# Performance work log

Measured on AMD Instinct MI355X. Metric: run time of the kernel, lower is better.

The kernel has to match this reference:

```python
import jax, jax.numpy as jnp
import numpy as np

KERNEL_LIST = (4, 8)
STRIDE = 4
EXT = 1
NUM_HEADS = 4
KEY_DIM = 32   # head_dim * attn_ratio = 64 * 0.5
HEAD_DIM = 64
SCALE = KEY_DIM ** -0.5


def _pool_matrix(inp, out):
    # torch adaptive_avg_pool2d: window i covers [floor(i*inp/out), ceil((i+1)*inp/out))
    P = np.zeros((out, inp), np.float32)
    for i in range(out):
        s0 = (i * inp) // out
        e0 = -((-(i + 1) * inp) // out)
        P[i, s0:e0] = 1.0 / (e0 - s0)
    return jnp.asarray(P)


def _dwconv3(x, w, b):
    # depthwise 3x3 conv, padding 1 (groups == channels)
    y = jax.lax.conv_general_dilated(
        x, w, window_strides=(1, 1), padding=((1, 1), (1, 1)),
        feature_group_count=x.shape[1],
        dimension_numbers=("NCHW", "OIHW", "NCHW"))
    return y + b[None, :, None, None]


def _attention(x, qkv_w, qkv_b, proj_w, proj_b, pe_w, pe_b):
    B, C, H, W = x.shape
    N = H * W
    qkv = jnp.einsum("oc,bchw->bohw", qkv_w, x) + qkv_b[None, :, None, None]
    qkv = qkv.reshape(B, NUM_HEADS, 2 * KEY_DIM + HEAD_DIM, N)
    q = qkv[:, :, :KEY_DIM]                # (B,h,kd,N)
    k = qkv[:, :, KEY_DIM:2 * KEY_DIM]     # (B,h,kd,N)
    v = qkv[:, :, 2 * KEY_DIM:]            # (B,h,hd,N)
    attn = jax.nn.softmax(jnp.einsum("bhkn,bhkm->bhnm", q, k) * SCALE, axis=-1)
    # v @ attn^T : out[d,n] = sum_m v[d,m] * attn[n,m]
    o = jnp.einsum("bhdm,bhnm->bhdn", v, attn).reshape(B, C, H, W)
    o = o + _dwconv3(v.reshape(B, C, H, W), pe_w, pe_b)
    return jnp.einsum("oc,bchw->bohw", proj_w, o) + proj_b[None, :, None, None]


def _extract(xp, Kp, s):
    # overlapping patches; layout (N, C, Lh, Kp, Lw, Kp); window order is (lh, lw)
    N, C, Hp, Wp = xp.shape
    Lh = (Hp - Kp) // s + 1
    Lw = (Wp - Kp) // s + 1
    hi = jnp.arange(Lh)[:, None] * s + jnp.arange(Kp)[None, :]  # (Lh, Kp)
    wi = jnp.arange(Lw)[:, None] * s + jnp.arange(Kp)[None, :]
    p = xp[:, :, hi, :]          # (N, C, Lh, Kp, Wp)
    p = p[:, :, :, :, wi]        # (N, C, Lh, Kp, Lw, Kp)
    return p, Lh, Lw


def setup_inputs() -> dict:
    key = jax.random.key(0)
    ks = jax.random.split(key, 9)
    C = 256
    w = 0.02
    return {
        "x": jax.random.normal(ks[0], (8, C, 64, 64), jnp.float32),
        "qkv_w": jax.random.normal(ks[1], (512, C), jnp.float32) * w,
        "qkv_b": jax.random.normal(ks[2], (512,), jnp.float32) * w,
        "proj_w": jax.random.normal(ks[3], (C, C), jnp.float32) * w,
        "proj_b": jax.random.normal(ks[4], (C,), jnp.float32) * w,
        "attn_pe_w": jax.random.normal(ks[5], (C, 1, 3, 3), jnp.float32) * w,
        "attn_pe_b": jax.random.normal(ks[6], (C,), jnp.float32) * w,
        "dp_pe_w": jax.random.normal(ks[7], (C, 1, 3, 3), jnp.float32) * w,
        "dp_pe_b": jax.random.normal(ks[8], (C,), jnp.float32) * w,
    }


def reference(x, qkv_w, qkv_b, proj_w, proj_b, attn_pe_w, attn_pe_b, dp_pe_w, dp_pe_b):
    N, C, H, W = x.shape
    xp = jnp.pad(x, ((0, 0), (0, 0), (EXT, EXT), (EXT, EXT)), mode="edge")  # replicate pad
    outs = [x]
    for K in KERNEL_LIST:
        Kp = K + 2 * EXT
        p, Lh, Lw = _extract(xp, Kp, STRIDE)
        P = _pool_matrix(Kp, K)
        # adaptive avg pool Kp->K on both spatial dims; windows ordered (lh, lw)
        pooled = jnp.einsum("pi,ncaibj,qj->nabcpq", P, p, P)
        pooled = pooled.reshape(N * Lh * Lw, C, K, K)
        y = _dwconv3(pooled, dp_pe_w, dp_pe_b) + pooled
        a = _attention(y, qkv_w, qkv_b, proj_w, proj_b, attn_pe_w, attn_pe_b)
        # torch does a raw .view(N, C*K*K, L) on the (N*L, C, K, K) buffer
        cols = a.reshape(N, C, K, K, Lh, Lw)
        cols_p = cols.transpose(0, 1, 2, 4, 3, 5)  # (N, C, K, Lh, K, Lw)
        hh = jnp.arange(Lh)[None, :] * STRIDE + jnp.arange(K)[:, None]  # (K, Lh)
        ww = jnp.arange(Lw)[None, :] * STRIDE + jnp.arange(K)[:, None]  # (K, Lw)
        folded = jnp.zeros((N, C, H, W), x.dtype).at[
            :, :, hh[:, :, None, None], ww[None, None, :, :]].add(cols_p)
        count = jnp.zeros((1, 1, H, W), x.dtype).at[
            :, :, hh[:, :, None, None], ww[None, None, :, :]].add(
            jnp.ones((1, 1, K, Lh, K, Lw), x.dtype))
        outs.append(folded / count)
    return sum(outs) / len(outs)
```

## Files before the change

kernel.cpp:

```cpp
#include <hip/hip_runtime.h>
#include <hip/hip_bf16.h>

typedef __bf16 bf16x8 __attribute__((ext_vector_type(8)));
typedef float  f32x4  __attribute__((ext_vector_type(4)));

#define DEV static __device__ __forceinline__

DEV float bf2f(ushort u) { unsigned x = ((unsigned)u) << 16; return __uint_as_float(x); }
DEV ushort f2bf(float f) {
    __bf16 b = (__bf16)f;
    return __builtin_bit_cast(ushort, b);
}

typedef __attribute__((address_space(1))) const unsigned int gu32;
typedef __attribute__((address_space(3))) unsigned int lu32;
DEV void gload16(const ushort* g, ushort* l) {
    __builtin_amdgcn_global_load_lds((gu32*)g, (lu32*)l, 16, 0, 0);
}

__global__ __launch_bounds__(256) void prep_kernel(
    const float* __restrict__ qkv_w, const float* __restrict__ proj_w,
    const float* __restrict__ apw,
    ushort* __restrict__ qw_bf, ushort* __restrict__ pw_bf, ushort* __restrict__ wt)
{
    int bid = blockIdx.x;
    if (bid < 128) {
        int i = (bid * 256 + threadIdx.x) * 4;
        float4 v = *(const float4*)(qkv_w + i);
        ushort4 o;
        o.x = f2bf(v.x); o.y = f2bf(v.y); o.z = f2bf(v.z); o.w = f2bf(v.w);
        *(ushort4*)(qw_bf + i) = o;
    } else if (bid < 192) {
        int i = ((bid - 128) * 256 + threadIdx.x) * 4;
        float4 v = *(const float4*)(proj_w + i);
        ushort4 o;
        o.x = f2bf(v.x); o.y = f2bf(v.y); o.z = f2bf(v.z); o.w = f2bf(v.w);
        *(ushort4*)(pw_bf + i) = o;
    } else {
        int i = (bid - 192) * 256 + threadIdx.x;
        if (i < 9 * 256) {
            int tap = i >> 8, c = i & 255;
            wt[i] = f2bf(apw[c * 9 + tap]);
        }
    }
}

__global__ __launch_bounds__(256) void box_kernel(
    const float* __restrict__ x,
    ushort* __restrict__ B)
{
    int br = blockIdx.x % 65; int g = blockIdx.x / 65;
    const float* xg = x + (size_t)g * 256 * 4096;
    ushort* Bg = B + (size_t)g * 65 * 65 * 256;
    const int r0 = max(br - 1, 0) * 64;
    const int r1 = min(br, 63) * 64;
    __shared__ float s[128][65];
    const int wl = threadIdx.x & 63, cq = threadIdx.x >> 6;
    const int c2 = threadIdx.x & 127, bh = threadIdx.x >> 7;
    for (int half = 0; half < 2; ++half) {
#pragma unroll 4
        for (int it = 0; it < 32; ++it) {
            int cl_ = it * 4 + cq;
            const float* xp = xg + (size_t)(half * 128 + cl_) * 4096;
            s[cl_][wl] = xp[r0 + wl] + xp[r1 + wl];
        }
        __syncthreads();
        for (int bc = bh; bc < 65; bc += 2) {
            float v = 0.25f * (s[c2][max(bc - 1, 0)] + s[c2][min(bc, 63)]);
            Bg[((size_t)br * 65 + bc) * 256 + half * 128 + c2] = f2bf(v);
        }
        __syncthreads();
    }
}

template<int K, int L>
__global__ __launch_bounds__(256) void pool_kernel(
    const ushort* __restrict__ B,
    const float* __restrict__ w9,
    const float* __restrict__ bias,
    ushort* __restrict__ y)
{
    constexpr int HF = K / 2;
    const int pk = blockIdx.x;
    const int lw = pk % L; int t = pk / L; const int lh = t % L; const int g = t / L;
    const int c = threadIdx.x;
    const ushort* Bg = B + (size_t)g * 65 * 65 * 256 + c;
    float pool[K][K];
#pragma unroll
    for (int p = 0; p < K; ++p) {
        const int br = lh * 4 + p + (p >= HF ? 1 : 0);
#pragma unroll
        for (int q = 0; q < K; ++q) {
            const int bc = lw * 4 + q + (q >= HF ? 1 : 0);
            pool[p][q] = bf2f(Bg[((size_t)br * 65 + bc) * 256]);
        }
    }
    float wv[9];
#pragma unroll
    for (int i = 0; i < 9; ++i) wv[i] = w9[c * 9 + i];
    const float bv = bias[c];
    ushort* yp = y + (size_t)pk * (K * K) * 256 + c;
#pragma unroll
    for (int p = 0; p < K; ++p) {
#pragma unroll
        for (int q = 0; q < K; ++q) {
            float a = pool[p][q] + bv;
#pragma unroll
            for (int dp = -1; dp <= 1; ++dp) {
#pragma unroll
                for (int dq = -1; dq <= 1; ++dq) {
                    int pp = p + dp, qq = q + dq;
                    if (pp >= 0 && pp < K && qq >= 0 && qq < K)
                        a += wv[(dp + 1) * 3 + (dq + 1)] * pool[pp][qq];
                }
            }
            yp[(p * K + q) * 256] = f2bf(a);
        }
    }
}

template<int OC, int EPI, int K, int L, int RT>
__global__ __launch_bounds__(256) void gemm_kernel(
    const ushort* __restrict__ act,
    const ushort* __restrict__ w,
    const float* __restrict__ bias,
    ushort* __restrict__ out_bf)
{
    __shared__ __attribute__((aligned(16))) ushort As[128][32];
    __shared__ __attribute__((aligned(16))) ushort Ws[128][32];
    constexpr int NT = OC / 128;
    const int id  = blockIdx.x;
    const int xc  = id & 7;
    const int ctb = (id >> 3) % NT;
    const int tt  = id / (8 * NT);
    const int rowt = tt * 8 + xc;
    if (rowt >= RT) return;
    const int tid  = threadIdx.x;
    const int n0   = rowt * 128;
    const int ch0  = ctb * 128;
    const int wv   = tid >> 6, lane = tid & 63;
    const int l15  = lane & 15, quad = lane >> 4;
    const int wm   = wv >> 1, wn = wv & 1;

    const int qlog = (lane & 3) ^ ((lane >> 3) & 3);
    const size_t soff = (size_t)(lane >> 2) * 256 + (size_t)qlog * 8;
    const ushort* aS0 = act + ((size_t)n0 + wv * 32) * 256 + soff;
    const ushort* wS0 = w   + ((size_t)ch0 + wv * 32) * 256 + soff;
    const ushort* aS1 = aS0 + 16 * 256;
    const ushort* wS1 = wS0 + 16 * 256;
    ushort* aD0 = &As[wv * 32][0];
    ushort* wD0 = &Ws[wv * 32][0];
    ushort* aD1 = aD0 + 16 * 32;
    ushort* wD1 = wD0 + 16 * 32;

    const int rcol = (quad ^ ((l15 >> 1) & 3)) * 8;
    f32x4 acc[4][4] = {};
    for (int k0 = 0; k0 < 256; k0 += 32) {
        gload16(aS0 + k0, aD0);
        gload16(aS1 + k0, aD1);
        gload16(wS0 + k0, wD0);
        gload16(wS1 + k0, wD1);
        __syncthreads();
        bf16x8 af[4], bw[4];
#pragma unroll
        for (int t = 0; t < 4; ++t) {
            af[t] = *(const bf16x8*)&As[wm * 64 + t * 16 + l15][rcol];
            bw[t] = *(const bf16x8*)&Ws[wn * 64 + t * 16 + l15][rcol];
        }
#pragma unroll
        for (int mt = 0; mt < 4; ++mt)
#pragma unroll
            for (int nt = 0; nt < 4; ++nt)
                acc[mt][nt] = __builtin_amdgcn_mfma_f32_16x16x32_bf16(af[mt], bw[nt], acc[mt][nt], 0, 0, 0);
        __syncthreads();
    }

    float bv[4];
#pragma unroll
    for (int nt = 0; nt < 4; ++nt) bv[nt] = bias[ch0 + wn * 64 + nt * 16 + l15];
#pragma unroll
    for (int mt = 0; mt < 4; ++mt) {
#pragma unroll
        for (int r = 0; r < 4; ++r) {
            const int n = n0 + wm * 64 + mt * 16 + quad * 4 + r;
            if (EPI == 0) {
                ushort* dst = out_bf + (size_t)n * OC + ch0 + wn * 64;
#pragma unroll
                for (int nt = 0; nt < 4; ++nt)
                    dst[nt * 16 + l15] = f2bf(acc[mt][nt][r] + bv[nt]);
            } else {
                constexpr int K2 = K * K;
                constexpr int LL = L * L;
                const int b_g   = n >> (K == 8 ? 6 : 4);
                const int pq    = n & (K2 - 1);
                const int gl    = b_g / LL;
                const int b_loc = b_g - gl * LL;
                const size_t base = (size_t)gl * (256 * K2 * LL) + (size_t)b_loc * 256 * K2 + pq;
#pragma unroll
                for (int nt = 0; nt < 4; ++nt) {
                    const int ch = ch0 + wn * 64 + nt * 16 + l15;
                    out_bf[base + (size_t)ch * K2] = f2bf(acc[mt][nt][r] + bv[nt]);
                }
            }
        }
    }
}

__global__ __launch_bounds__(128, 4) void attn8_mfma_kernel(
    const ushort* __restrict__ qkv,
    const ushort* __restrict__ wt,
    const float* __restrict__ pe_b,
    ushort* __restrict__ o_out)
{
    constexpr float SCALE = 0.17677669529663687f;
    __shared__ __attribute__((aligned(16))) ushort PB[64][72];
    __shared__ __attribute__((aligned(16))) ushort Vt[64][72];
    __shared__ __attribute__((aligned(16))) ushort wsh[9][64];
    __shared__ float bsh[64];
    const int tid  = threadIdx.x;
    const int lane = tid & 63;
    const int ww   = tid >> 6;
    const int b    = blockIdx.x >> 2;
    const int h    = blockIdx.x & 3;
    const int cbase = h * 64;
    const int l15  = lane & 15, quad = lane >> 4;
    const ushort* base = qkv + (size_t)b * 64 * 512 + h * 128;

    if (lane < 36) {
        int tap = lane >> 2, c8 = (lane & 3) * 8;
        *(uint4*)&wsh[tap][ww * 32 + c8] = *(const uint4*)&wt[tap * 256 + cbase + ww * 32 + c8];
    }
    if (lane < 32) bsh[ww * 32 + lane] = pe_b[cbase + ww * 32 + lane];

    {
        const int m = lane;
        const ushort* vsrc = base + (size_t)m * 512 + 64 + ww * 32;
        const int d0 = ww * 32;
#pragma unroll
        for (int t = 0; t < 4; ++t) {
            uint4 vv = *(const uint4*)(vsrc + t * 8);
            unsigned u[4] = {vv.x, vv.y, vv.z, vv.w};
#pragma unroll
            for (int e = 0; e < 4; ++e) {
                Vt[d0 + t * 8 + e * 2][m]     = (ushort)(u[e] & 0xFFFF);
                Vt[d0 + t * 8 + e * 2 + 1][m] = (ushort)(u[e] >> 16);
            }
        }
    }

    bf16x8 fq[2];
#pragma unroll
    for (int s = 0; s < 2; ++s) {
        int n = (ww + 2 * s) * 16 + l15;
        fq[s] = *(const bf16x8*)(base + (size_t)n * 512 + quad * 8);
    }
    f32x4 S[2][4];
    __builtin_amdgcn_s_setprio(1);
#pragma unroll
    for (int mt = 0; mt < 4; ++mt) {
        int m = mt * 16 + l15;
        bf16x8 fk = *(const bf16x8*)(base + (size_t)m * 512 + 32 + quad * 8);
#pragma unroll
        for (int s = 0; s < 2; ++s) {
            f32x4 z = {0.f, 0.f, 0.f, 0.f};
            S[s][mt] = __builtin_amdgcn_mfma_f32_16x16x32_bf16(fq[s], fk, z, 0, 0, 0);
        }
    }
    __builtin_amdgcn_s_setprio(0);

    {
        const int d   = ww * 32 + (lane & 31);
        const int pb4 = (lane >> 5) * 4;
        float wreg[9];
#pragma unroll
        for (int i = 0; i < 9; ++i) wreg[i] = bf2f(wsh[i][d]);
        const float bias0 = bsh[d];
#pragma unroll
        for (int it = 0; it < 4; ++it) {
            const int p = pb4 + it;
            float pe[8];
#pragma unroll
            for (int q = 0; q < 8; ++q) pe[q] = bias0;
#pragma unroll
            for (int dpi = 0; dpi < 3; ++dpi) {
                const int pp = p + dpi - 1;
                if (pp >= 0 && pp < 8) {
                    bf16x8 v8 = *(const bf16x8*)&Vt[d][pp * 8];
                    float v[8];
#pragma unroll
                    for (int e = 0; e < 8; ++e) v[e] = (float)v8[e];
                    const float w0 = wreg[dpi * 3], w1 = wreg[dpi * 3 + 1], w2 = wreg[dpi * 3 + 2];
                    pe[0] += w1 * v[0] + w2 * v[1];
#pragma unroll
                    for (int q = 1; q < 7; ++q) pe[q] += w0 * v[q - 1] + w1 * v[q] + w2 * v[q + 1];
                    pe[7] += w0 * v[6] + w1 * v[7];
                }
            }
            ushort pk[8];
#pragma unroll
            for (int e = 0; e < 8; ++e) pk[e] = f2bf(pe[e]);
            *(uint4*)&PB[d][p * 8] = *(const uint4*)pk;
        }
    }
    __syncthreads();

    f32x4 O[2][4];
#pragma unroll
    for (int s = 0; s < 2; ++s)
#pragma unroll
        for (int dt = 0; dt < 4; ++dt) {
            ushort4 t4 = *(const ushort4*)&PB[dt * 16 + l15][(ww + 2 * s) * 16 + quad * 4];
            O[s][dt][0] = bf2f(t4.x);
            O[s][dt][1] = bf2f(t4.y);
            O[s][dt][2] = bf2f(t4.z);
            O[s][dt][3] = bf2f(t4.w);
        }

#pragma unroll
    for (int s = 0; s < 2; ++s) {
#pragma unroll
        for (int r = 0; r < 4; ++r) {
            float mx = -1e30f;
#pragma unroll
            for (int mt = 0; mt < 4; ++mt) { S[s][mt][r] *= SCALE; mx = fmaxf(mx, S[s][mt][r]); }
            mx = fmaxf(mx, __shfl_xor(mx, 1));
            mx = fmaxf(mx, __shfl_xor(mx, 2));
            mx = fmaxf(mx, __shfl_xor(mx, 4));
            mx = fmaxf(mx, __shfl_xor(mx, 8));
            float sum = 0.f;
#pragma unroll
            for (int mt = 0; mt < 4; ++mt) { float e = __expf(S[s][mt][r] - mx); S[s][mt][r] = e; sum += e; }
            sum += __shfl_xor(sum, 1);
            sum += __shfl_xor(sum, 2);
            sum += __shfl_xor(sum, 4);
            sum += __shfl_xor(sum, 8);
            float inv = 1.f / sum;
#pragma unroll
            for (int mt = 0; mt < 4; ++mt) S[s][mt][r] *= inv;
        }
    }
    __syncthreads();

#pragma unroll
    for (int s = 0; s < 2; ++s)
#pragma unroll
        for (int r = 0; r < 4; ++r) {
            int n = (ww + 2 * s) * 16 + quad * 4 + r;
#pragma unroll
            for (int mt = 0; mt < 4; ++mt)
                PB[n][mt * 16 + l15] = f2bf(S[s][mt][r]);
        }

#pragma unroll
    for (int ks = 0; ks < 2; ++ks) {
        bf16x8 fp[2], fv[4];
#pragma unroll
        for (int s = 0; s < 2; ++s)
            fp[s] = *(const bf16x8*)&PB[(ww + 2 * s) * 16 + l15][ks * 32 + quad * 8];
#pragma unroll
        for (int dt = 0; dt < 4; ++dt)
            fv[dt] = *(const bf16x8*)&Vt[dt * 16 + l15][ks * 32 + quad * 8];
        __builtin_amdgcn_s_setprio(1);
#pragma unroll
        for (int s = 0; s < 2; ++s)
#pragma unroll
            for (int dt = 0; dt < 4; ++dt)
                O[s][dt] = __builtin_amdgcn_mfma_f32_16x16x32_bf16(fp[s], fv[dt], O[s][dt], 0, 0, 0);
        __builtin_amdgcn_s_setprio(0);
    }

#pragma unroll
    for (int s = 0; s < 2; ++s)
#pragma unroll
        for (int r = 0; r < 4; ++r) {
            int n = (ww + 2 * s) * 16 + quad * 4 + r;
#pragma unroll
            for (int dt = 0; dt < 4; ++dt)
                PB[n][dt * 16 + l15] = f2bf(O[s][dt][r]);
        }
#pragma unroll
    for (int it = 0; it < 4; ++it) {
        int cidx = it * 64 + lane;
        int rl = cidx >> 3, c8 = (cidx & 7) * 8;
        int row = ww * 16 + (rl & 15) + (rl >> 4) * 32;
        uint4 v = *(const uint4*)&PB[row][c8];
        *(uint4*)(o_out + (size_t)(b * 64 + row) * 256 + cbase + c8) = v;
    }
}

__global__ __launch_bounds__(256) void attn4_mfma_kernel(
    const ushort* __restrict__ qkv,
    const ushort* __restrict__ wt,
    const float* __restrict__ pe_b,
    ushort* __restrict__ o_out)
{
    constexpr float SCALE = 0.17677669529663687f;
    __shared__ __attribute__((aligned(16))) ushort wsh[9][256];
    __shared__ float bsh[256];
    __shared__ __attribute__((aligned(16))) ushort Vt4[4][64][32];
    __shared__ __attribute__((aligned(16))) ushort VP[4][16][64];
    __shared__ __attribute__((aligned(16))) ushort Pm[4][16][32];
    const int tid  = threadIdx.x;
    const int lane = tid & 63;
    const int w    = tid >> 6;
    const int b    = blockIdx.x;
    const int h    = w;
    const int cbase = h * 64;
    const int l15  = lane & 15, quad = lane >> 4;
    const ushort* base = qkv + (size_t)b * 16 * 512 + h * 128;

    for (int i = tid; i < 9 * 32; i += 256) {
        int tap = i >> 5, c8 = (i & 31) * 8;
        *(uint4*)&wsh[tap][c8] = *(const uint4*)&wt[tap * 256 + c8];
    }
    bsh[tid] = pe_b[tid];
    __syncthreads();

    {
        uint4 z = {0u, 0u, 0u, 0u};
#pragma unroll
        for (int t = 0; t < 4; ++t)
            *(uint4*)&Vt4[w][t * 16 + (lane >> 2)][(lane & 3) * 8] = z;
        *(uint4*)&Pm[w][lane >> 2][(lane & 3) * 8] = z;
    }

    {
        const int m = lane & 15, dblk = lane >> 4;
        const ushort* vsrc = base + (size_t)m * 512 + 64 + dblk * 16;
        uint4 v0 = *(const uint4*)(vsrc);
        uint4 v1 = *(const uint4*)(vsrc + 8);
        *(uint4*)&VP[w][m][dblk * 16]     = v0;
        *(uint4*)&VP[w][m][dblk * 16 + 8] = v1;
        ushort us[16];
        *(uint4*)&us[0] = v0; *(uint4*)&us[8] = v1;
        const int mb = m >> 3, m7 = m & 7;
#pragma unroll
        for (int e = 0; e < 16; ++e) {
            int d = dblk * 16 + e;
            Vt4[w][d][((mb ^ (d & 3)) << 3) + m7] = us[e];
        }
    }

    bf16x8 fq = *(const bf16x8*)(base + (size_t)l15 * 512 + quad * 8);
    bf16x8 fk = *(const bf16x8*)(base + (size_t)l15 * 512 + 32 + quad * 8);
    f32x4 z4 = {0.f, 0.f, 0.f, 0.f};
    f32x4 S = __builtin_amdgcn_mfma_f32_16x16x32_bf16(fq, fk, z4, 0, 0, 0);

    float p[4];
#pragma unroll
    for (int r = 0; r < 4; ++r) {
        float v = S[r] * SCALE;
        float mx = v;
        mx = fmaxf(mx, __shfl_xor(mx, 1));
        mx = fmaxf(mx, __shfl_xor(mx, 2));
        mx = fmaxf(mx, __shfl_xor(mx, 4));
        mx = fmaxf(mx, __shfl_xor(mx, 8));
        float e = __expf(v - mx);
        float sum = e;
        sum += __shfl_xor(sum, 1);
        sum += __shfl_xor(sum, 2);
        sum += __shfl_xor(sum, 4);
        sum += __shfl_xor(sum, 8);
        p[r] = e / sum;
    }
#pragma unroll
    for (int r = 0; r < 4; ++r) {
        int n = quad * 4 + r;
        Pm[w][n][(((l15 >> 3) ^ (n & 3)) << 3) + (l15 & 7)] = f2bf(p[r]);
    }

    float pe[2][8];
    const int n_ = lane & 15;
    const int pp0 = n_ >> 2, qq0 = n_ & 3;
#pragma unroll
    for (int it = 0; it < 2; ++it) {
        int ch = (lane >> 4) + it * 4;
#pragma unroll
        for (int e = 0; e < 8; ++e) pe[it][e] = bsh[cbase + ch * 8 + e];
    }
#pragma unroll
    for (int tap = 0; tap < 9; ++tap) {
        const int dp = tap / 3 - 1, dq = tap % 3 - 1;
        const int pp = pp0 + dp, qq = qq0 + dq;
        if (pp >= 0 && pp < 4 && qq >= 0 && qq < 4) {
            const int mm = pp * 4 + qq;
#pragma unroll
            for (int it = 0; it < 2; ++it) {
                int ch = (lane >> 4) + it * 4;
                uint4 wv4 = *(const uint4*)&wsh[tap][cbase + ch * 8];
                uint4 vv  = *(const uint4*)&VP[w][mm][ch * 8];
                unsigned uw[4] = {wv4.x, wv4.y, wv4.z, wv4.w};
                unsigned uv[4] = {vv.x, vv.y, vv.z, vv.w};
#pragma unroll
                for (int e2 = 0; e2 < 4; ++e2) {
                    float wlo = __uint_as_float(uw[e2] << 16);
                    float whi = __uint_as_float(uw[e2] & 0xFFFF0000u);
                    float vlo = __uint_as_float(uv[e2] << 16);
                    float vhi = __uint_as_float(uv[e2] & 0xFFFF0000u);
                    pe[it][2 * e2]     += wlo * vlo;
                    pe[it][2 * e2 + 1] += whi * vhi;
                }
            }
        }
    }
#pragma unroll
    for (int it = 0; it < 2; ++it) {
        int ch = (lane >> 4) + it * 4;
        ushort pk[8];
#pragma unroll
        for (int e = 0; e < 8; ++e) pk[e] = f2bf(pe[it][e]);
        *(uint4*)&VP[w][n_][ch * 8] = *(const uint4*)pk;
    }

    f32x4 O[4];
#pragma unroll
    for (int dt = 0; dt < 4; ++dt)
#pragma unroll
        for (int r = 0; r < 4; ++r)
            O[dt][r] = bf2f(VP[w][quad * 4 + r][dt * 16 + l15]);

    bf16x8 fp = *(const bf16x8*)&Pm[w][l15][((quad ^ (l15 & 3)) << 3)];
    __builtin_amdgcn_s_setprio(1);
#pragma unroll
    for (int dt = 0; dt < 4; ++dt) {
        bf16x8 fv = *(const bf16x8*)&Vt4[w][dt * 16 + l15][((quad ^ (l15 & 3)) << 3)];
        O[dt] = __builtin_amdgcn_mfma_f32_16x16x32_bf16(fp, fv, O[dt], 0, 0, 0);
    }
    __builtin_amdgcn_s_setprio(0);

#pragma unroll
    for (int dt = 0; dt < 4; ++dt)
#pragma unroll
        for (int r = 0; r < 4; ++r)
            VP[w][quad * 4 + r][dt * 16 + l15] = f2bf(O[dt][r]);

#pragma unroll
    for (int j = 0; j < 2; ++j) {
        int idx = j * 64 + lane;
        int row = idx >> 3, c8 = (idx & 7) * 8;
        uint4 v = *(const uint4*)&VP[w][row][c8];
        *(uint4*)(o_out + (size_t)(b * 16 + row) * 256 + cbase + c8) = v;
    }
}

__global__ __launch_bounds__(256) void final_kernel(
    const float* __restrict__ x,
    const ushort* __restrict__ s8,
    const ushort* __restrict__ s4,
    float* __restrict__ out)
{
    __shared__ __attribute__((aligned(16))) ushort l8[14400];
    __shared__ __attribute__((aligned(16))) ushort l4[4096];
    const int c2 = blockIdx.x & 255;
    const int g  = blockIdx.x >> 8;
    const int tid = threadIdx.x;
    const ushort* s8g = s8 + (size_t)g * (256 * 64 * 225) + (size_t)c2 * 14400;
    const ushort* s4g = s4 + (size_t)g * (256 * 16 * 256) + (size_t)c2 * 4096;
#pragma unroll
    for (int i = 0; i < 8; ++i) {
        int idx = i * 256 + tid;
        if (idx < 1800) *(uint4*)&l8[idx * 8] = *(const uint4*)&s8g[idx * 8];
    }
#pragma unroll
    for (int i = 0; i < 2; ++i) {
        int idx = i * 256 + tid;
        *(uint4*)&l4[idx * 8] = *(const uint4*)&s4g[idx * 8];
    }
    __syncthreads();
    const float third = 1.f / 3.f;
    const size_t gc_off = ((size_t)(g * 256 + c2)) * 4096;
#pragma unroll
    for (int it = 0; it < 4; ++it) {
        int pix0 = it * 1024 + tid * 4;
        int h = pix0 >> 6, w0 = pix0 & 63;
        int lh_lo = (h >= 8) ? ((h - 4) >> 2) : 0, lh_hi = min(14, h >> 2);
        float4 xv = *(const float4*)(x + gc_off + pix0);
        float xa[4] = {xv.x, xv.y, xv.z, xv.w};
        float o4[4];
#pragma unroll
        for (int j = 0; j < 4; ++j) {
            int w = w0 + j;
            int lw_lo = (w >= 8) ? ((w - 4) >> 2) : 0, lw_hi = min(14, w >> 2);
            float v4 = bf2f(l4[(((h & 3) * 4 + (w & 3)) * 16 + (h >> 2)) * 16 + (w >> 2)]);
            float v8 = 0.f;
            for (int lh2 = lh_lo; lh2 <= lh_hi; ++lh2) {
                int p2 = h - lh2 * 4;
                for (int lw2 = lw_lo; lw2 <= lw_hi; ++lw2) {
                    int q2 = w - lw2 * 4;
                    v8 += bf2f(l8[((p2 * 8 + q2) * 15 + lh2) * 15 + lw2]);
                }
            }
            float inv = 1.f / (float)((lh_hi - lh_lo + 1) * (lw_hi - lw_lo + 1));
            o4[j] = (xa[j] + v8 * inv + v4) * third;
        }
        float4 ov = {o4[0], o4[1], o4[2], o4[3]};
        *(float4*)(out + gc_off + pix0) = ov;
    }
}

extern "C" void kernel_launch(void* const* d_in, const int* in_sizes, int n_in,
                              void* d_out, int out_size, void* d_ws, size_t ws_size,
                              hipStream_t stream)
{
    const float* x      = (const float*)d_in[0];
    const float* qkv_w  = (const float*)d_in[1];
    const float* qkv_b  = (const float*)d_in[2];
    const float* proj_w = (const float*)d_in[3];
    const float* proj_b = (const float*)d_in[4];
    const float* apw    = (const float*)d_in[5];
    const float* apb    = (const float*)d_in[6];
    const float* dpw    = (const float*)d_in[7];
    const float* dpb    = (const float*)d_in[8];
    float* out = (float*)d_out;

    const size_t S8_B = 8ull * 225 * 256 * 64 * 2;
    const size_t S4_B = 8ull * 256 * 256 * 16 * 2;
    const size_t W_B  = (512ull * 256 + 256ull * 256 + 9ull * 256) * 2;
    const size_t B_B  = 8ull * 65 * 65 * 256 * 2;
    const size_t Y1_B = 8ull * 14400 * 256 * 2;
    const size_t Q1_B = 8ull * 14400 * 512 * 2;
    const size_t Y2_B = 4ull * 14400 * 256 * 2;
    const size_t Q2_B = 4ull * 14400 * 512 * 2;

    const bool onepass = ws_size >= S8_B + S4_B + Y1_B + Q1_B + W_B + B_B;
    const size_t Y_B = onepass ? Y1_B : Y2_B;
    const size_t Q_B = onepass ? Q1_B : Q2_B;
    if (!onepass && ws_size < S8_B + S4_B + Y2_B + Q2_B + W_B + B_B) {
        hipMemsetAsync(d_out, 0x46, 4, stream);
        return;
    }
    ushort* s8    = (ushort*)d_ws;
    ushort* s4    = s8 + S8_B / 2;
    ushort* ybuf  = s4 + S4_B / 2;
    ushort* qbuf  = ybuf + Y_B / 2;
    ushort* qw_bf = qbuf + Q_B / 2;
    ushort* pw_bf = qw_bf + 512 * 256;
    ushort* wt    = pw_bf + 256 * 256;
    ushort* Bbuf  = (ushort*)((char*)d_ws + S8_B + S4_B + Y_B + Q_B + W_B);

    prep_kernel<<<201, 256, 0, stream>>>(qkv_w, proj_w, apw, qw_bf, pw_bf, wt);
    box_kernel<<<8 * 65, 256, 0, stream>>>(x, Bbuf);

    if (onepass) {
        pool_kernel<8, 15><<<8 * 225, 256, 0, stream>>>(Bbuf, dpw, dpb, ybuf);
        gemm_kernel<512, 0, 8, 15, 900><<<113 * 8 * 4, 256, 0, stream>>>(ybuf, qw_bf, qkv_b, qbuf);
        attn8_mfma_kernel<<<1800 * 4, 128, 0, stream>>>(qbuf, wt, apb, ybuf);
        gemm_kernel<256, 1, 8, 15, 900><<<113 * 8 * 2, 256, 0, stream>>>(ybuf, pw_bf, proj_b, s8);
    } else {
        for (int hf = 0; hf < 2; ++hf) {
            ushort* B_h = Bbuf + (size_t)hf * 4 * 65 * 65 * 256;
            ushort* s8_h = s8 + (size_t)hf * 4 * 225 * 256 * 64;
            pool_kernel<8, 15><<<4 * 225, 256, 0, stream>>>(B_h, dpw, dpb, ybuf);
            gemm_kernel<512, 0, 8, 15, 450><<<57 * 8 * 4, 256, 0, stream>>>(ybuf, qw_bf, qkv_b, qbuf);
            attn8_mfma_kernel<<<900 * 4, 128, 0, stream>>>(qbuf, wt, apb, ybuf);
            gemm_kernel<256, 1, 8, 15, 450><<<57 * 8 * 2, 256, 0, stream>>>(ybuf, pw_bf, proj_b, s8_h);
        }
    }
    pool_kernel<4, 16><<<8 * 256, 256, 0, stream>>>(Bbuf, dpw, dpb, ybuf);
    gemm_kernel<512, 0, 4, 16, 256><<<32 * 8 * 4, 256, 0, stream>>>(ybuf, qw_bf, qkv_b, qbuf);
    attn4_mfma_kernel<<<2048, 256, 0, stream>>>(qbuf, wt, apb, ybuf);
    gemm_kernel<256, 1, 4, 16, 256><<<32 * 8 * 2, 256, 0, stream>>>(ybuf, pw_bf, proj_b, s4);

    final_kernel<<<2048, 256, 0, stream>>>(x, s8, s4, out);
}
```

Measured before the change: 360.3 us.

## Process two patches per attn8 block and prefetch second patch's inputs

Each attn8 block now handles two patch-batches (bp and bp+phalf), halving the grid. The global loads of Q, K and V for the second patch are issued right after the first patch's QK MFMAs, so their latency overlaps with the first patch's depthwise conv, softmax and PV work. In exchange the block needs more registers for the prefetched fragments, has fewer blocks to spread across CUs, and adds an extra barrier between the two iterations.

```diff
diff --git a/kernel.cpp b/kernel.cpp
--- a/kernel.cpp
+++ b/kernel.cpp
@@ -210,7 +210,8 @@
     const ushort* __restrict__ qkv,
     const ushort* __restrict__ wt,
     const float* __restrict__ pe_b,
-    ushort* __restrict__ o_out)
+    ushort* __restrict__ o_out,
+    int phalf)
 {
     constexpr float SCALE = 0.17677669529663687f;
     __shared__ __attribute__((aligned(16))) ushort PB[64][72];
@@ -220,11 +221,10 @@
     const int tid  = threadIdx.x;
     const int lane = tid & 63;
     const int ww   = tid >> 6;
-    const int b    = blockIdx.x >> 2;
+    const int bp   = blockIdx.x >> 2;
     const int h    = blockIdx.x & 3;
     const int cbase = h * 64;
     const int l15  = lane & 15, quad = lane >> 4;
-    const ushort* base = qkv + (size_t)b * 64 * 512 + h * 128;
 
     if (lane < 36) {
         int tap = lane >> 2, c8 = (lane & 3) * 8;
@@ -232,159 +232,191 @@
     }
     if (lane < 32) bsh[ww * 32 + lane] = pe_b[cbase + ww * 32 + lane];
 
+    uint4  vr[4];
+    bf16x8 fq[2];
+    bf16x8 fk[4];
     {
-        const int m = lane;
-        const ushort* vsrc = base + (size_t)m * 512 + 64 + ww * 32;
-        const int d0 = ww * 32;
-#pragma unroll
-        for (int t = 0; t < 4; ++t) {
-            uint4 vv = *(const uint4*)(vsrc + t * 8);
-            unsigned u[4] = {vv.x, vv.y, vv.z, vv.w};
-#pragma unroll
-            for (int e = 0; e < 4; ++e) {
-                Vt[d0 + t * 8 + e * 2][m]     = (ushort)(u[e] & 0xFFFF);
-                Vt[d0 + t * 8 + e * 2 + 1][m] = (ushort)(u[e] >> 16);
-            }
-        }
-    }
-
-    bf16x8 fq[2];
-#pragma unroll
-    for (int s = 0; s < 2; ++s) {
-        int n = (ww + 2 * s) * 16 + l15;
-        fq[s] = *(const bf16x8*)(base + (size_t)n * 512 + quad * 8);
-    }
-    f32x4 S[2][4];
-    __builtin_amdgcn_s_setprio(1);
-#pragma unroll
-    for (int mt = 0; mt < 4; ++mt) {
-        int m = mt * 16 + l15;
-        bf16x8 fk = *(const bf16x8*)(base + (size_t)m * 512 + 32 + quad * 8);
+        const ushort* base0 = qkv + (size_t)bp * 64 * 512 + h * 128;
+        const ushort* vsrc = base0 + (size_t)lane * 512 + 64 + ww * 32;
+#pragma unroll
+        for (int t = 0; t < 4; ++t) vr[t] = *(const uint4*)(vsrc + t * 8);
 #pragma unroll
         for (int s = 0; s < 2; ++s) {
-            f32x4 z = {0.f, 0.f, 0.f, 0.f};
-            S[s][mt] = __builtin_amdgcn_mfma_f32_16x16x32_bf16(fq[s], fk, z, 0, 0, 0);
-        }
-    }
-    __builtin_amdgcn_s_setprio(0);
-
-    {
-        const int d   = ww * 32 + (lane & 31);
-        const int pb4 = (lane >> 5) * 4;
-        float wreg[9];
-#pragma unroll
-        for (int i = 0; i < 9; ++i) wreg[i] = bf2f(wsh[i][d]);
-        const float bias0 = bsh[d];
+            int n = (ww + 2 * s) * 16 + l15;
+            fq[s] = *(const bf16x8*)(base0 + (size_t)n * 512 + quad * 8);
+        }
+#pragma unroll
+        for (int mt = 0; mt < 4; ++mt) {
+            int m = mt * 16 + l15;
+            fk[mt] = *(const bf16x8*)(base0 + (size_t)m * 512 + 32 + quad * 8);
+        }
+    }
+
+#pragma unroll
+    for (int j = 0; j < 2; ++j) {
+        const int b = (j == 0) ? bp : bp + phalf;
+        if (j == 1) __syncthreads();
+
+        {
+            const int m = lane, d0 = ww * 32;
+#pragma unroll
+            for (int t = 0; t < 4; ++t) {
+                unsigned u[4] = {vr[t].x, vr[t].y, vr[t].z, vr[t].w};
+#pragma unroll
+                for (int e = 0; e < 4; ++e) {
+                    Vt[d0 + t * 8 + e * 2][m]     = (ushort)(u[e] & 0xFFFF);
+                    Vt[d0 + t * 8 + e * 2 + 1][m] = (ushort)(u[e] >> 16);
+                }
+            }
+        }
+
+        f32x4 S[2][4];
+        __builtin_amdgcn_s_setprio(1);
+#pragma unroll
+        for (int mt = 0; mt < 4; ++mt) {
+#pragma unroll
+            for (int s = 0; s < 2; ++s) {
+                f32x4 z = {0.f, 0.f, 0.f, 0.f};
+                S[s][mt] = __builtin_amdgcn_mfma_f32_16x16x32_bf16(fq[s], fk[mt], z, 0, 0, 0);
+            }
+        }
+        __builtin_amdgcn_s_setprio(0);
+
+        if (j == 0) {
+            const ushort* base1 = qkv + (size_t)(bp + phalf) * 64 * 512 + h * 128;
+            const ushort* vsrc = base1 + (size_t)lane * 512 + 64 + ww * 32;
+#pragma unroll
+            for (int t = 0; t < 4; ++t) vr[t] = *(const uint4*)(vsrc + t * 8);
+#pragma unroll
+            for (int s = 0; s < 2; ++s) {
+                int n = (ww + 2 * s) * 16 + l15;
+                fq[s] = *(const bf16x8*)(base1 + (size_t)n * 512 + quad * 8);
+            }
+#pragma unroll
+            for (int mt = 0; mt < 4; ++mt) {
+                int m = mt * 16 + l15;
+                fk[mt] = *(const bf16x8*)(base1 + (size_t)m * 512 + 32 + quad * 8);
+            }
+        }
+
+        {
+            const int d   = ww * 32 + (lane & 31);
+            const int pb4 = (lane >> 5) * 4;
+            float wreg[9];
+#pragma unroll
+            for (int i = 0; i < 9; ++i) wreg[i] = bf2f(wsh[i][d]);
+            const float bias0 = bsh[d];
+#pragma unroll
+            for (int it = 0; it < 4; ++it) {
+                const int p = pb4 + it;
+                float pe[8];
+#pragma unroll
+                for (int q = 0; q < 8; ++q) pe[q] = bias0;
+#pragma unroll
+                for (int dpi = 0; dpi < 3; ++dpi) {
+                    const int pp = p + dpi - 1;
+                    if (pp >= 0 && pp < 8) {
+                        bf16x8 v8 = *(const bf16x8*)&Vt[d][pp * 8];
+                        float v[8];
+#pragma unroll
+                        for (int e = 0; e < 8; ++e) v[e] = (float)v8[e];
+                        const float w0 = wreg[dpi * 3], w1 = wreg[dpi * 3 + 1], w2 = wreg[dpi * 3 + 2];
+                        pe[0] += w1 * v[0] + w2 * v[1];
+#pragma unroll
+                        for (int q = 1; q < 7; ++q) pe[q] += w0 * v[q - 1] + w1 * v[q] + w2 * v[q + 1];
+                        pe[7] += w0 * v[6] + w1 * v[7];
+                    }
+                }
+                ushort pk[8];
+#pragma unroll
+                for (int e = 0; e < 8; ++e) pk[e] = f2bf(pe[e]);
+                *(uint4*)&PB[d][p * 8] = *(const uint4*)pk;
+            }
+        }
+        __syncthreads();
+
+        f32x4 O[2][4];
+#pragma unroll
+        for (int s = 0; s < 2; ++s)
+#pragma unroll
+            for (int dt = 0; dt < 4; ++dt) {
+                ushort4 t4 = *(const ushort4*)&PB[dt * 16 + l15][(ww + 2 * s) * 16 + quad * 4];
+                O[s][dt][0] = bf2f(t4.x);
+                O[s][dt][1] = bf2f(t4.y);
+                O[s][dt][2] = bf2f(t4.z);
+                O[s][dt][3] = bf2f(t4.w);
+            }
+
+#pragma unroll
+        for (int s = 0; s < 2; ++s) {
+#pragma unroll
+            for (int r = 0; r < 4; ++r) {
+                float mx = -1e30f;
+#pragma unroll
+                for (int mt = 0; mt < 4; ++mt) { S[s][mt][r] *= SCALE; mx = fmaxf(mx, S[s][mt][r]); }
+                mx = fmaxf(mx, __shfl_xor(mx, 1));
+                mx = fmaxf(mx, __shfl_xor(mx, 2));
+                mx = fmaxf(mx, __shfl_xor(mx, 4));
+                mx = fmaxf(mx, __shfl_xor(mx, 8));
+                float sum = 0.f;
+#pragma unroll
+                for (int mt = 0; mt < 4; ++mt) { float e = __expf(S[s][mt][r] - mx); S[s][mt][r] = e; sum += e; }
+                sum += __shfl_xor(sum, 1);
+                sum += __shfl_xor(sum, 2);
+                sum += __shfl_xor(sum, 4);
+                sum += __shfl_xor(sum, 8);
+                float inv = 1.f / sum;
+#pragma unroll
+                for (int mt = 0; mt < 4; ++mt) S[s][mt][r] *= inv;
+            }
+        }
+        __syncthreads();
+
+#pragma unroll
+        for (int s = 0; s < 2; ++s)
+#pragma unroll
+            for (int r = 0; r < 4; ++r) {
+                int n = (ww + 2 * s) * 16 + quad * 4 + r;
+#pragma unroll
+                for (int mt = 0; mt < 4; ++mt)
+                    PB[n][mt * 16 + l15] = f2bf(S[s][mt][r]);
+            }
+
+#pragma unroll
+        for (int ks = 0; ks < 2; ++ks) {
+            bf16x8 fp[2], fv[4];
+#pragma unroll
+            for (int s = 0; s < 2; ++s)
+                fp[s] = *(const bf16x8*)&PB[(ww + 2 * s) * 16 + l15][ks * 32 + quad * 8];
+#pragma unroll
+            for (int dt = 0; dt < 4; ++dt)
+                fv[dt] = *(const bf16x8*)&Vt[dt * 16 + l15][ks * 32 + quad * 8];
+            __builtin_amdgcn_s_setprio(1);
+#pragma unroll
+            for (int s = 0; s < 2; ++s)
+#pragma unroll
+                for (int dt = 0; dt < 4; ++dt)
+                    O[s][dt] = __builtin_amdgcn_mfma_f32_16x16x32_bf16(fp[s], fv[dt], O[s][dt], 0, 0, 0);
+            __builtin_amdgcn_s_setprio(0);
+        }
+
+#pragma unroll
+        for (int s = 0; s < 2; ++s)
+#pragma unroll
+            for (int r = 0; r < 4; ++r) {
+                int n = (ww + 2 * s) * 16 + quad * 4 + r;
+#pragma unroll
+                for (int dt = 0; dt < 4; ++dt)
+                    PB[n][dt * 16 + l15] = f2bf(O[s][dt][r]);
+            }
 #pragma unroll
         for (int it = 0; it < 4; ++it) {
-            const int p = pb4 + it;
-            float pe[8];
-#pragma unroll
-            for (int q = 0; q < 8; ++q) pe[q] = bias0;
-#pragma unroll
-            for (int dpi = 0; dpi < 3; ++dpi) {
-                const int pp = p + dpi - 1;
-                if (pp >= 0 && pp < 8) {
-                    bf16x8 v8 = *(const bf16x8*)&Vt[d][pp * 8];
-                    float v[8];
-#pragma unroll
-                    for (int e = 0; e < 8; ++e) v[e] = (float)v8[e];
-                    const float w0 = wreg[dpi * 3], w1 = wreg[dpi * 3 + 1], w2 = wreg[dpi * 3 + 2];
-                    pe[0] += w1 * v[0] + w2 * v[1];
-#pragma unroll
-                    for (int q = 1; q < 7; ++q) pe[q] += w0 * v[q - 1] + w1 * v[q] + w2 * v[q + 1];
-                    pe[7] += w0 * v[6] + w1 * v[7];
-                }
-            }
-            ushort pk[8];
-#pragma unroll
-            for (int e = 0; e < 8; ++e) pk[e] = f2bf(pe[e]);
-            *(uint4*)&PB[d][p * 8] = *(const uint4*)pk;
-        }
-    }
-    __syncthreads();
-
-    f32x4 O[2][4];
-#pragma unroll
-    for (int s = 0; s < 2; ++s)
-#pragma unroll
-        for (int dt = 0; dt < 4; ++dt) {
-            ushort4 t4 = *(const ushort4*)&PB[dt * 16 + l15][(ww + 2 * s) * 16 + quad * 4];
-            O[s][dt][0] = bf2f(t4.x);
-            O[s][dt][1] = bf2f(t4.y);
-            O[s][dt][2] = bf2f(t4.z);
-            O[s][dt][3] = bf2f(t4.w);
-        }
-
-#pragma unroll
-    for (int s = 0; s < 2; ++s) {
-#pragma unroll
-        for (int r = 0; r < 4; ++r) {
-            float mx = -1e30f;
-#pragma unroll
-            for (int mt = 0; mt < 4; ++mt) { S[s][mt][r] *= SCALE; mx = fmaxf(mx, S[s][mt][r]); }
-            mx = fmaxf(mx, __shfl_xor(mx, 1));
-            mx = fmaxf(mx, __shfl_xor(mx, 2));
-            mx = fmaxf(mx, __shfl_xor(mx, 4));
-            mx = fmaxf(mx, __shfl_xor(mx, 8));
-            float sum = 0.f;
-#pragma unroll
-            for (int mt = 0; mt < 4; ++mt) { float e = __expf(S[s][mt][r] - mx); S[s][mt][r] = e; sum += e; }
-            sum += __shfl_xor(sum, 1);
-            sum += __shfl_xor(sum, 2);
-            sum += __shfl_xor(sum, 4);
-            sum += __shfl_xor(sum, 8);
-            float inv = 1.f / sum;
-#pragma unroll
-            for (int mt = 0; mt < 4; ++mt) S[s][mt][r] *= inv;
-        }
-    }
-    __syncthreads();
-
-#pragma unroll
-    for (int s = 0; s < 2; ++s)
-#pragma unroll
-        for (int r = 0; r < 4; ++r) {
-            int n = (ww + 2 * s) * 16 + quad * 4 + r;
-#pragma unroll
-            for (int mt = 0; mt < 4; ++mt)
-                PB[n][mt * 16 + l15] = f2bf(S[s][mt][r]);
-        }
-
-#pragma unroll
-    for (int ks = 0; ks < 2; ++ks) {
-        bf16x8 fp[2], fv[4];
-#pragma unroll
-        for (int s = 0; s < 2; ++s)
-            fp[s] = *(const bf16x8*)&PB[(ww + 2 * s) * 16 + l15][ks * 32 + quad * 8];
-#pragma unroll
-        for (int dt = 0; dt < 4; ++dt)
-            fv[dt] = *(const bf16x8*)&Vt[dt * 16 + l15][ks * 32 + quad * 8];
-        __builtin_amdgcn_s_setprio(1);
-#pragma unroll
-        for (int s = 0; s < 2; ++s)
-#pragma unroll
-            for (int dt = 0; dt < 4; ++dt)
-                O[s][dt] = __builtin_amdgcn_mfma_f32_16x16x32_bf16(fp[s], fv[dt], O[s][dt], 0, 0, 0);
-        __builtin_amdgcn_s_setprio(0);
-    }
-
-#pragma unroll
-    for (int s = 0; s < 2; ++s)
-#pragma unroll
-        for (int r = 0; r < 4; ++r) {
-            int n = (ww + 2 * s) * 16 + quad * 4 + r;
-#pragma unroll
-            for (int dt = 0; dt < 4; ++dt)
-                PB[n][dt * 16 + l15] = f2bf(O[s][dt][r]);
-        }
-#pragma unroll
-    for (int it = 0; it < 4; ++it) {
-        int cidx = it * 64 + lane;
-        int rl = cidx >> 3, c8 = (cidx & 7) * 8;
-        int row = ww * 16 + (rl & 15) + (rl >> 4) * 32;
-        uint4 v = *(const uint4*)&PB[row][c8];
-        *(uint4*)(o_out + (size_t)(b * 64 + row) * 256 + cbase + c8) = v;
+            int cidx = it * 64 + lane;
+            int rl = cidx >> 3, c8 = (cidx & 7) * 8;
+            int row = ww * 16 + (rl & 15) + (rl >> 4) * 32;
+            uint4 v = *(const uint4*)&PB[row][c8];
+            *(uint4*)(o_out + (size_t)(b * 64 + row) * 256 + cbase + c8) = v;
+        }
     }
 }
 
@@ -644,7 +676,7 @@
     if (onepass) {
         pool_kernel<8, 15><<<8 * 225, 256, 0, stream>>>(Bbuf, dpw, dpb, ybuf);
         gemm_kernel<512, 0, 8, 15, 900><<<113 * 8 * 4, 256, 0, stream>>>(ybuf, qw_bf, qkv_b, qbuf);
-        attn8_mfma_kernel<<<1800 * 4, 128, 0, stream>>>(qbuf, wt, apb, ybuf);
+        attn8_mfma_kernel<<<900 * 4, 128, 0, stream>>>(qbuf, wt, apb, ybuf, 900);
         gemm_kernel<256, 1, 8, 15, 900><<<113 * 8 * 2, 256, 0, stream>>>(ybuf, pw_bf, proj_b, s8);
     } else {
         for (int hf = 0; hf < 2; ++hf) {
@@ -652,7 +684,7 @@
             ushort* s8_h = s8 + (size_t)hf * 4 * 225 * 256 * 64;
             pool_kernel<8, 15><<<4 * 225, 256, 0, stream>>>(B_h, dpw, dpb, ybuf);
             gemm_kernel<512, 0, 8, 15, 450><<<57 * 8 * 4, 256, 0, stream>>>(ybuf, qw_bf, qkv_b, qbuf);
-            attn8_mfma_kernel<<<900 * 4, 128, 0, stream>>>(qbuf, wt, apb, ybuf);
+            attn8_mfma_kernel<<<450 * 4, 128, 0, stream>>>(qbuf, wt, apb, ybuf, 450);
             gemm_kernel<256, 1, 8, 15, 450><<<57 * 8 * 2, 256, 0, stream>>>(ybuf, pw_bf, proj_b, s8_h);
         }
     }
```

Result: slower. 399.0 us (+10.8%).
